# Kernel tuning notes

Hardware: AMD Instinct MI355X
Metric: run time of the kernel (lower is better)

## Reference

```python
import jax, jax.numpy as jnp
import numpy as np

HIDDEN = 128
N_RBF = 32
LMAX = 2
N_NODES = 10000
DEG = 8  # each node has DEG outgoing (and DEG incoming) edges on a ring


def _build_graph():
    src = np.repeat(np.arange(N_NODES, dtype=np.int64), DEG)
    offs = np.tile(np.arange(1, DEG + 1, dtype=np.int64), N_NODES)
    dst = (src + offs) % N_NODES
    keys = src * N_NODES + dst
    order = np.argsort(keys)
    src2, dst2 = src[order], dst[order]  # e2 sorted by key (searchsorted invariant)
    e1_to_e2 = np.empty_like(order)
    e1_to_e2[order] = np.arange(order.size)
    return src, dst, src2, dst2, e1_to_e2


def setup_inputs() -> dict:
    key = jax.random.key(0)
    ks = jax.random.split(key, 12)
    src1, dst1, src2, dst2, e1_to_e2 = _build_graph()
    E1, E2 = src1.size, src2.size
    in_dim = 6 * HIDDEN + 3 * N_RBF + 1  # 865

    def lin(k, fi, fo):
        kw, kb = jax.random.split(k)
        s = 1.0 / np.sqrt(fi)
        return (jax.random.uniform(kw, (fi, fo), minval=-s, maxval=s),
                jax.random.uniform(kb, (fo,), minval=-s, maxval=s))

    w1, b1 = lin(ks[0], in_dim, HIDDEN)
    w2, b2 = lin(ks[1], HIDDEN, HIDDEN)
    wgw, bgw = lin(ks[2], HIDDEN, HIDDEN)
    wgt, bgt = lin(ks[3], HIDDEN, HIDDEN)
    return {
        "t_e2": jax.random.normal(ks[4], (E2, HIDDEN), dtype=jnp.float32),
        "h": jax.random.normal(ks[5], (N_NODES, HIDDEN), dtype=jnp.float32),
        "edge_index1": jnp.asarray(np.stack([src1, dst1])),
        "edge_index2": jnp.asarray(np.stack([src2, dst2])),
        "e1_to_e2": jnp.asarray(e1_to_e2),
        "dist_e1": jax.random.uniform(ks[6], (E1,), dtype=jnp.float32),
        "dist_e2": jax.random.uniform(ks[7], (E2,), dtype=jnp.float32),
        "rbf_e1": jax.random.normal(ks[8], (E1, N_RBF), dtype=jnp.float32),
        "rbf_e2": jax.random.normal(ks[9], (E2, N_RBF), dtype=jnp.float32),
        "sph_e1": jax.random.normal(ks[10], (E1, LMAX + 1), dtype=jnp.float32),
        "num_nodes": N_NODES,
        "w1": w1, "b1": b1, "w2": w2, "b2": b2,
        "wgw": wgw, "bgw": bgw, "wgt": wgt, "bgt": bgt,
    }


def _wedge_indices(edge_index1, edge_index2, num_nodes):
    """Host-side (numpy, vectorized) wedge construction: for every center node k,
    all (incoming edge i->k, outgoing edge k->j) pairs with i != j, kept only when
    (i, j) itself is an edge in e2 (looked up by sorted key search)."""
    src1 = np.asarray(edge_index1[0]); dst1 = np.asarray(edge_index1[1])
    src2 = np.asarray(edge_index2[0]); dst2 = np.asarray(edge_index2[1])
    nz = src1 != dst1  # drop self-loops
    s, d = src1[nz], dst1[nz]
    eid = np.nonzero(nz)[0]
    out_deg = np.bincount(s, minlength=num_nodes)
    out_order = np.argsort(s, kind="stable")  # filtered-edge positions grouped by src
    out_ptr = np.concatenate([np.zeros(1, np.int64), np.cumsum(out_deg)])
    reps = out_deg[d]  # each incoming edge pairs with out_deg[center] outgoing edges
    total = int(reps.sum())
    if total == 0:
        z = np.zeros(0, np.int64)
        return z, z, z, z, z, z
    starts = np.cumsum(reps) - reps
    local = np.arange(total) - np.repeat(starts, reps)
    kj_f = out_order[np.repeat(out_ptr[d], reps) + local]
    i = np.repeat(s, reps)
    k = np.repeat(d, reps)
    eik = np.repeat(eid, reps)
    j = d[kj_f]
    ekj = eid[kj_f]
    m = i != j
    i, k, j, eik, ekj = i[m], k[m], j[m], eik[m], ekj[m]
    e2_keys = src2.astype(np.int64) * num_nodes + dst2
    pk = i.astype(np.int64) * num_nodes + j
    pos = np.searchsorted(e2_keys, pk)
    posc = np.minimum(pos, e2_keys.size - 1)
    valid = (pos < e2_keys.size) & (e2_keys[posc] == pk)
    return i[valid], k[valid], j[valid], eik[valid], ekj[valid], posc[valid]


def reference(t_e2, h, edge_index1, edge_index2, e1_to_e2, dist_e1, dist_e2,
              rbf_e1, rbf_e2, sph_e1, num_nodes,
              w1, b1, w2, b2, wgw, bgw, wgt, bgt):
    i, k, j, eik, ekj, eij = _wedge_indices(edge_index1, edge_index2, int(num_nodes))
    if i.size == 0:
        return t_e2
    i, k, j = jnp.asarray(i), jnp.asarray(k), jnp.asarray(j)
    eik, ekj, eij = jnp.asarray(eik), jnp.asarray(ekj), jnp.asarray(eij)
    e1e2 = jnp.asarray(e1_to_e2)
    # wedge geometric features (wedge_use_high_degree=False -> l=1 contraction only)
    c_feat = (sph_e1[eik, 1] * sph_e1[ekj, 1])[:, None]           # [W, 1]
    g = jnp.concatenate([rbf_e1[eik], rbf_e1[ekj], rbf_e2[eij], c_feat], axis=-1)
    rho_in = jnp.concatenate([t_e2[e1e2[eik]], t_e2[e1e2[ekj]], t_e2[eij],
                              h[i], h[k], h[j], g], axis=-1)       # [W, 865]
    msg = jax.nn.silu(rho_in @ w1 + b1) @ w2 + b2                  # [W, H]
    m = jax.ops.segment_sum(msg, eij, num_segments=t_e2.shape[0])  # [E2, H]
    return t_e2 + jax.nn.sigmoid(m @ wgw + bgw) * jnp.tanh(t_e2 @ wgt + bgt)
```

## Files before the change

kernel.cpp:

```cpp
#include <hip/hip_runtime.h>
#include <math.h>

typedef unsigned short u16;
typedef unsigned int u32;
typedef __bf16 bf16x8 __attribute__((ext_vector_type(8)));
typedef float f32x4 __attribute__((ext_vector_type(4)));

__device__ __forceinline__ float bf2f(u16 v){ union{u32 u;float f;}c; c.u=((u32)v)<<16; return c.f; }
__device__ __forceinline__ u16 f2bf(float f){ union{__bf16 h; u16 u;}c; c.h=(__bf16)f; return c.u; }
__device__ __forceinline__ u32 pk2(float a, float b){
  union{ __bf16 h[2]; u32 u; }c; c.h[0]=(__bf16)a; c.h[1]=(__bf16)b; return c.u;
}
__device__ __forceinline__ uint4 ld8f(const float* p){
  float4 x = ((const float4*)p)[0];
  float4 y = ((const float4*)p)[1];
  uint4 r; r.x=pk2(x.x,x.y); r.y=pk2(x.z,x.w); r.z=pk2(y.x,y.y); r.w=pk2(y.z,y.w);
  return r;
}
__device__ __forceinline__ float fsilu(float x){
  return x*__builtin_amdgcn_rcpf(1.f+__expf(-x));
}

__global__ void k_setup_all(const int* __restrict__ e1_to_e2,
                            const float* __restrict__ rbf_e1,
                            const float* __restrict__ sph_e1,
                            u16* __restrict__ rbf1p, float* __restrict__ sph_c, int E1,
                            const int* __restrict__ src2, int* __restrict__ out_ptr,
                            int Nn, int E2,
                            const float* __restrict__ w1,
                            u16* __restrict__ W0T, u16* __restrict__ W1T,
                            u16* __restrict__ W2T,
                            const float* __restrict__ w2, const float* __restrict__ wgw,
                            const float* __restrict__ wgt, const float* __restrict__ b2,
                            u16* __restrict__ WcT, u16* __restrict__ WgtT,
                            float* __restrict__ bc2,
                            int nb0, int nb1, int nb2) {
  const int b = blockIdx.x, t = threadIdx.x;
  if (b < nb0) {
    int e = b*256 + t;
    if (e >= E1) return;
    int f = e1_to_e2[e];
    sph_c[f] = sph_e1[e*3+1];
    const float* s = rbf_e1 + (size_t)e*32;
    uint4* d = (uint4*)(rbf1p + (size_t)f*32);
    d[0]=ld8f(s); d[1]=ld8f(s+8); d[2]=ld8f(s+16); d[3]=ld8f(s+24);
  } else if (b < nb1) {
    int n = (b-nb0)*256 + t;
    if (n > Nn) return;
    int lo=0, hi=E2;
    while (lo<hi){ int m=(lo+hi)>>1; if (src2[m]<n) lo=m+1; else hi=m; }
    out_ptr[n]=lo;
  } else if (b < nb2) {
    int id = (b-nb1)*256 + t;
    if (id < 128*416) {
      int n = id/416, k = id - n*416;
      int row = (k<128)? k : (k<256)? 384+(k-128) : (k<384)? 512+(k-256) : 768+(k-384);
      W0T[id] = f2bf(w1[row*128+n]);
    } else if (id < 128*(416+288)) {
      int id2 = id - 128*416;
      int n = id2/288, k = id2 - n*288;
      int row = (k<128)? 128+k : (k<256)? 640+(k-128) : 800+(k-256);
      W1T[id2] = f2bf(w1[row*128+n]);
    } else if (id < 128*864) {
      int id2 = id - 128*704;
      int n = id2/160, k = id2 - n*160;
      int row = (k<128)? 256+k : 832+(k-128);
      W2T[id2] = f2bf(w1[row*128+n]);
    }
  } else {
    int id = (b-nb2)*256 + t;
    if (id < 16384) {
      int n = id&127, k = id>>7;
      float s = 0.f;
      for (int r=0;r<128;r++) s += w2[k*128+r]*wgw[r*128+n];
      WcT[n*128+k] = f2bf(s);
      WgtT[n*128+k] = f2bf(wgt[k*128+n]);
    } else if (id < 16384+128) {
      int n = id-16384;
      float s = 0.f;
      for (int r=0;r<128;r++) s += b2[r]*wgw[r*128+n];
      bc2[n] = s;
    }
  }
}

__global__ __launch_bounds__(256, 8)
void k_wedge(const int* __restrict__ src2, const int* __restrict__ dst2,
             const int* __restrict__ out_ptr, const float* __restrict__ sph_c,
             const u16* __restrict__ Q1, const u16* __restrict__ Q2,
             const u16* __restrict__ P3, const float* __restrict__ w1,
             u16* __restrict__ S, int* __restrict__ cnt, int E2) {
  int gw = (int)((blockIdx.x*256 + threadIdx.x) >> 6);
  int lane = threadIdx.x & 63;
  if (gw >= E2) return;
  int i = src2[gw], j = dst2[gw];
  int f = 0, lo = 0; float cf = 0.f; bool valid = false;
  if (lane < 8) {
    int ff = out_ptr[i] + lane;
    if (ff < out_ptr[i+1]) {
      int k = dst2[ff];
      int l = out_ptr[k], hh = out_ptr[k+1], h0 = hh;
      while (l<hh){ int m=(l+hh)>>1; if (dst2[m]<j) l=m+1; else hh=m; }
      if (l<h0 && dst2[l]==j){ valid=true; f=ff; lo=l; cf=sph_c[ff]*sph_c[l]; }
    }
  }
  unsigned long long mask = __ballot(valid);
  const int nw = __popcll(mask);
  if (lane==0) cnt[gw] = nw;
  u32 p3u = ((const u32*)(P3 + (size_t)gw*128))[lane];
  float p30 = bf2f((u16)(p3u&0xffff)), p31 = bf2f((u16)(p3u>>16));
  float2 wv = ((const float2*)(w1 + 864*128))[lane];
  const u32* q1b = (const u32*)Q1;
  const u32* q2b = (const u32*)Q2;

  u32 xa[8], ya[8]; float ca[8];
  unsigned long long m2 = mask;
  #pragma unroll
  for (int s=0; s<8; s++) {
    if (s < nw) {
      int b = __ffsll((long long)m2)-1; m2 &= m2-1;
      int fA = __builtin_amdgcn_readlane(f, b);
      int lA = __builtin_amdgcn_readlane(lo, b);
      ca[s] = __int_as_float(__builtin_amdgcn_readlane(__float_as_int(cf), b));
      xa[s] = q1b[((size_t)(u32)fA<<6) + lane];
      ya[s] = q2b[((size_t)(u32)lA<<6) + lane];
    }
  }

  float a0=0.f, a1=0.f;
  #pragma unroll
  for (int s=0; s<8; s++) {
    if (s < nw) {
      float b0 = fmaf(ca[s], wv.x, p30);
      float b1 = fmaf(ca[s], wv.y, p31);
      float x0 = b0 + bf2f((u16)(xa[s]&0xffff)) + bf2f((u16)(ya[s]&0xffff));
      float x1 = b1 + bf2f((u16)(xa[s]>>16))    + bf2f((u16)(ya[s]>>16));
      a0 += fsilu(x0);
      a1 += fsilu(x1);
    }
  }
  ((u32*)(S + (size_t)gw*128))[lane] = pk2(a0, a1);
}

struct GArgs {
  const float* t_f32; const float* h; const float* rbf_e2;
  const u16* rbf1p; const u16* Asrc;
  const int* src2; const int* dst2; const int* cnt;
  const u16* B0; const u16* B1; const u16* B2;
  const u16* Bmat; const u16* Bmat2;
  const float* b1; const float* bgw; const float* bgt; const float* bc2;
  u16* out0; u16* out1; u16* out2;
  float* outf;
  int M;
};

__global__ __launch_bounds__(256, 2)
void k_gemm0(GArgs a) {
  const int nwg = gridDim.x;
  const int id  = blockIdx.x;
  const int xcd = id & 7, idx = id >> 3;
  const int q = nwg >> 3, r = nwg & 7;
  const int w = (xcd < r ? xcd*(q+1) : r*(q+1) + (xcd-r)*q) + idx;
  const int bm = w/3, bn = w - bm*3;

  __shared__ u16 As[128*40];
  __shared__ u16 Bs[128*40];
  const int tid = threadIdx.x;
  const int lane = tid & 63, wave = tid >> 6;
  const int wm = wave >> 1, wn = wave & 1;
  const int quad = lane >> 4, l16 = lane & 15;

  const int part = tid & 3;
  const int ra = tid >> 2;
  const int rb = ra + 64;
  long fa = (long)bm*128 + ra;
  long fb = (long)bm*128 + rb;
  if (fa >= a.M) fa = a.M-1;
  if (fb >= a.M) fb = a.M-1;
  int sa=0, sb=0, da=0, db=0;
  if (bn==0) { sa=a.src2[fa]; sb=a.src2[fb]; }
  if (bn<2)  { da=a.dst2[fa]; db=a.dst2[fb]; }

  const u16* Bp = (bn==0)? a.B0 : (bn==1)? a.B1 : a.B2;
  const int NK = (bn==0)? 13 : (bn==1)? 9 : 5;
  const int KT = NK*32;

  f32x4 acc[4][4] = {};
  for (int ks=0; ks<NK; ks++) {
    const int kb = ks*32;
    uint4 va, vb;
    if (ks<4)                    { va = ld8f(a.t_f32 + fa*128 + kb + part*8);
                                   vb = ld8f(a.t_f32 + fb*128 + kb + part*8); }
    else if (bn==0 && ks<8)      { va = ld8f(a.h + (long)sa*128 + (kb-128) + part*8);
                                   vb = ld8f(a.h + (long)sb*128 + (kb-128) + part*8); }
    else if (bn==0 && ks<12)     { va = ld8f(a.h + (long)da*128 + (kb-256) + part*8);
                                   vb = ld8f(a.h + (long)db*128 + (kb-256) + part*8); }
    else if (bn==1 && ks<8)      { va = ld8f(a.h + (long)da*128 + (kb-128) + part*8);
                                   vb = ld8f(a.h + (long)db*128 + (kb-128) + part*8); }
    else if (bn==2)              { va = ld8f(a.rbf_e2 + fa*32 + part*8);
                                   vb = ld8f(a.rbf_e2 + fb*32 + part*8); }
    else                         { va = *(const uint4*)(a.rbf1p + fa*32 + part*8);
                                   vb = *(const uint4*)(a.rbf1p + fb*32 + part*8); }
    uint4 wa = *(const uint4*)(Bp + (long)ra*KT + kb + part*8);
    uint4 wb = *(const uint4*)(Bp + (long)rb*KT + kb + part*8);
    __syncthreads();
    *(uint4*)(As + ra*40 + part*8) = va;
    *(uint4*)(As + rb*40 + part*8) = vb;
    *(uint4*)(Bs + ra*40 + part*8) = wa;
    *(uint4*)(Bs + rb*40 + part*8) = wb;
    __syncthreads();
    bf16x8 af[4], bfr[4];
    #pragma unroll
    for (int t=0;t<4;t++) {
      af[t]  = *(const bf16x8*)(As + (wm*64 + t*16 + l16)*40 + quad*8);
      bfr[t] = *(const bf16x8*)(Bs + (wn*64 + t*16 + l16)*40 + quad*8);
    }
    #pragma unroll
    for (int tm=0;tm<4;tm++)
      #pragma unroll
      for (int tn=0;tn<4;tn++)
        acc[tm][tn] = __builtin_amdgcn_mfma_f32_16x16x32_bf16(af[tm], bfr[tn], acc[tm][tn], 0,0,0);
  }

  #pragma unroll
  for (int tm=0;tm<4;tm++) {
    const int rloc = wm*64 + tm*16 + quad*4;
    #pragma unroll
    for (int r=0;r<4;r++) {
      long row = (long)bm*128 + rloc + r;
      if (row >= a.M) continue;
      #pragma unroll
      for (int tn=0;tn<4;tn++) {
        const int col = wn*64 + tn*16 + l16;
        float v = acc[tm][tn][r];
        u16* dst = (bn==0)? a.out0 : (bn==1)? a.out1 : a.out2;
        if (bn==2) v += a.b1[col];
        dst[row*128 + col] = f2bf(v);
      }
    }
  }
}

__global__ __launch_bounds__(256, 2)
void k_gemm12(GArgs a) {
  __shared__ u16 As[128*40];
  __shared__ u16 Bs[128*40];
  const int tid = threadIdx.x;
  const int bm = blockIdx.x;
  const int lane = tid & 63, wave = tid >> 6;
  const int wm = wave >> 1, wn = wave & 1;
  const int quad = lane >> 4, l16 = lane & 15;

  const int part = tid & 3;
  const int ra = tid >> 2;
  const int rb = ra + 64;
  long fa = (long)bm*128 + ra;
  long fb = (long)bm*128 + rb;
  if (fa >= a.M) fa = a.M-1;
  if (fb >= a.M) fb = a.M-1;

  f32x4 acc1[4][4] = {};
  f32x4 acc2[4][4] = {};
  for (int ks=0; ks<4; ks++) {
    const int kb = ks*32;
    uint4 va = *(const uint4*)(a.Asrc + fa*128 + kb + part*8);
    uint4 vb = *(const uint4*)(a.Asrc + fb*128 + kb + part*8);
    uint4 wa = *(const uint4*)(a.Bmat + (long)ra*128 + kb + part*8);
    uint4 wbv= *(const uint4*)(a.Bmat + (long)rb*128 + kb + part*8);
    __syncthreads();
    *(uint4*)(As + ra*40 + part*8) = va;
    *(uint4*)(As + rb*40 + part*8) = vb;
    *(uint4*)(Bs + ra*40 + part*8) = wa;
    *(uint4*)(Bs + rb*40 + part*8) = wbv;
    __syncthreads();
    bf16x8 af[4], bfr[4];
    #pragma unroll
    for (int t=0;t<4;t++) {
      af[t]  = *(const bf16x8*)(As + (wm*64 + t*16 + l16)*40 + quad*8);
      bfr[t] = *(const bf16x8*)(Bs + (wn*64 + t*16 + l16)*40 + quad*8);
    }
    #pragma unroll
    for (int tm=0;tm<4;tm++)
      #pragma unroll
      for (int tn=0;tn<4;tn++)
        acc1[tm][tn] = __builtin_amdgcn_mfma_f32_16x16x32_bf16(af[tm], bfr[tn], acc1[tm][tn], 0,0,0);
  }
  for (int ks=0; ks<4; ks++) {
    const int kb = ks*32;
    uint4 va = ld8f(a.t_f32 + fa*128 + kb + part*8);
    uint4 vb = ld8f(a.t_f32 + fb*128 + kb + part*8);
    uint4 wa = *(const uint4*)(a.Bmat2 + (long)ra*128 + kb + part*8);
    uint4 wbv= *(const uint4*)(a.Bmat2 + (long)rb*128 + kb + part*8);
    __syncthreads();
    *(uint4*)(As + ra*40 + part*8) = va;
    *(uint4*)(As + rb*40 + part*8) = vb;
    *(uint4*)(Bs + ra*40 + part*8) = wa;
    *(uint4*)(Bs + rb*40 + part*8) = wbv;
    __syncthreads();
    bf16x8 af[4], bfr[4];
    #pragma unroll
    for (int t=0;t<4;t++) {
      af[t]  = *(const bf16x8*)(As + (wm*64 + t*16 + l16)*40 + quad*8);
      bfr[t] = *(const bf16x8*)(Bs + (wn*64 + t*16 + l16)*40 + quad*8);
    }
    #pragma unroll
    for (int tm=0;tm<4;tm++)
      #pragma unroll
      for (int tn=0;tn<4;tn++)
        acc2[tm][tn] = __builtin_amdgcn_mfma_f32_16x16x32_bf16(af[tm], bfr[tn], acc2[tm][tn], 0,0,0);
  }

  #pragma unroll
  for (int tm=0;tm<4;tm++) {
    const int rloc = wm*64 + tm*16 + quad*4;
    #pragma unroll
    for (int r=0;r<4;r++) {
      long row = (long)bm*128 + rloc + r;
      if (row >= a.M) continue;
      #pragma unroll
      for (int tn=0;tn<4;tn++) {
        const int col = wn*64 + tn*16 + l16;
        float u = acc1[tm][tn][r] + (float)a.cnt[row]*a.bc2[col] + a.bgw[col];
        float g = __builtin_amdgcn_rcpf(1.f+__expf(-u));
        float vv = acc2[tm][tn][r] + a.bgt[col];
        float th = 1.f - 2.f*__builtin_amdgcn_rcpf(__expf(2.f*vv)+1.f);
        float t  = a.t_f32[row*128+col];
        a.outf[row*128+col] = t + g*th;
      }
    }
  }
}

extern "C" void kernel_launch(void* const* d_in, const int* in_sizes, int n_in,
                              void* d_out, int out_size, void* d_ws, size_t ws_size,
                              hipStream_t stream) {
  const float* t_e2  = (const float*)d_in[0];
  const float* h     = (const float*)d_in[1];
  const int* ei2     = (const int*)d_in[3];
  const int* e1_to_e2 = (const int*)d_in[4];
  const float* rbf_e1 = (const float*)d_in[7];
  const float* rbf_e2 = (const float*)d_in[8];
  const float* sph_e1 = (const float*)d_in[9];
  const float* w1  = (const float*)d_in[11];
  const float* b1  = (const float*)d_in[12];
  const float* w2  = (const float*)d_in[13];
  const float* b2  = (const float*)d_in[14];
  const float* wgw = (const float*)d_in[15];
  const float* bgw = (const float*)d_in[16];
  const float* wgt = (const float*)d_in[17];
  const float* bgt = (const float*)d_in[18];

  const int E2 = in_sizes[0]/128;
  const int Nn = in_sizes[1]/128;
  const int E1 = in_sizes[5];
  const int* src2 = ei2;
  const int* dst2 = ei2 + E2;

  char* p = (char*)d_ws;
  u16* Q1 = (u16*)p;       p += (size_t)E2*128*2;
  u16* Q2 = (u16*)p;       p += (size_t)E2*128*2;
  u16* P3 = (u16*)p;       p += (size_t)E2*128*2;
  u16* rbf1p = (u16*)p;    p += (size_t)E2*32*2;
  u16* W0T = (u16*)p;      p += (size_t)128*416*2;
  u16* W1T = (u16*)p;      p += (size_t)128*288*2;
  u16* W2T = (u16*)p;      p += (size_t)128*160*2;
  u16* WcT   = (u16*)p;    p += (size_t)128*128*2;
  u16* WgtT  = (u16*)p;    p += (size_t)128*128*2;
  float* sph_c = (float*)p; p += (size_t)E2*4;
  float* bc2   = (float*)p; p += 512;
  int* out_ptr = (int*)p;   p += (((size_t)(Nn+1)*4 + 63)/64)*64;
  int* cnt     = (int*)p;   p += (size_t)E2*4;
  u16* S = P3;

  const int nb_edges = (E1+255)/256;
  const int nb_ptr   = (Nn+1+255)/256;
  const int nb_w     = (128*864+255)/256;
  const int nb_small = (16512+255)/256;
  const int nb0 = nb_edges;
  const int nb1 = nb0 + nb_ptr;
  const int nb2 = nb1 + nb_w;
  const int nbT = nb2 + nb_small;
  k_setup_all<<<nbT, 256, 0, stream>>>(e1_to_e2, rbf_e1, sph_e1, rbf1p, sph_c, E1,
                                       src2, out_ptr, Nn, E2,
                                       w1, W0T, W1T, W2T,
                                       w2, wgw, wgt, b2,
                                       WcT, WgtT, bc2,
                                       nb0, nb1, nb2);

  const int Mb = (E2+127)/128;
  {
    GArgs a = {};
    a.t_f32=t_e2; a.h=h; a.rbf1p=rbf1p; a.rbf_e2=rbf_e2;
    a.src2=src2; a.dst2=dst2;
    a.B0=W0T; a.B1=W1T; a.B2=W2T; a.b1=b1;
    a.out0=Q1; a.out1=Q2; a.out2=P3; a.M=E2;
    k_gemm0<<<Mb*3, 256, 0, stream>>>(a);
  }
  k_wedge<<<(E2+3)/4, 256, 0, stream>>>(src2, dst2, out_ptr, sph_c,
                                        Q1, Q2, P3, w1, S, cnt, E2);
  {
    GArgs a = {};
    a.Asrc=S; a.cnt=cnt; a.Bmat=WcT; a.Bmat2=WgtT;
    a.bgw=bgw; a.bgt=bgt; a.bc2=bc2; a.t_f32=t_e2;
    a.outf=(float*)d_out; a.M=E2;
    k_gemm12<<<Mb, 256, 0, stream>>>(a);
  }
}
```

Baseline: 281.1 us.

## Double-buffer LDS tiles in gemm kernels to overlap global loads with MFMA

Both GEMM kernels now use two LDS buffers per operand, prefetching the next K-slice into registers while MFMAs consume the current slice, then writing it to the alternate buffer. This cuts one barrier per iteration and hides global load latency behind compute. k_gemm0 also raises launch_bounds min blocks from 2 to 4, which may pressure registers given the 64 accumulator floats plus prefetch registers, and doubled LDS (40KB per block) could limit occupancy.

```diff
diff --git a/kernel.cpp b/kernel.cpp
--- a/kernel.cpp
+++ b/kernel.cpp
@@ -154,7 +154,18 @@
   int M;
 };
 
-__global__ __launch_bounds__(256, 2)
+__device__ __forceinline__ uint4 ldA(const GArgs& a, int bn, int ks, long f,
+                                     int s, int d, int part) {
+  const int kb = ks*32;
+  if (ks<4)                return ld8f(a.t_f32 + f*128 + kb + part*8);
+  if (bn==0 && ks<8)       return ld8f(a.h + (long)s*128 + (kb-128) + part*8);
+  if (bn==0 && ks<12)      return ld8f(a.h + (long)d*128 + (kb-256) + part*8);
+  if (bn==1 && ks<8)       return ld8f(a.h + (long)d*128 + (kb-128) + part*8);
+  if (bn==2)               return ld8f(a.rbf_e2 + f*32 + part*8);
+  return *(const uint4*)(a.rbf1p + f*32 + part*8);
+}
+
+__global__ __launch_bounds__(256, 4)
 void k_gemm0(GArgs a) {
   const int nwg = gridDim.x;
   const int id  = blockIdx.x;
@@ -163,8 +174,8 @@
   const int w = (xcd < r ? xcd*(q+1) : r*(q+1) + (xcd-r)*q) + idx;
   const int bm = w/3, bn = w - bm*3;
 
-  __shared__ u16 As[128*40];
-  __shared__ u16 Bs[128*40];
+  __shared__ u16 As[2][128*40];
+  __shared__ u16 Bs[2][128*40];
   const int tid = threadIdx.x;
   const int lane = tid & 63, wave = tid >> 6;
   const int wm = wave >> 1, wn = wave & 1;
@@ -185,41 +196,43 @@
   const int NK = (bn==0)? 13 : (bn==1)? 9 : 5;
   const int KT = NK*32;
 
+  uint4 va = ldA(a,bn,0,fa,sa,da,part);
+  uint4 vb = ldA(a,bn,0,fb,sb,db,part);
+  uint4 wa = *(const uint4*)(Bp + (long)ra*KT + part*8);
+  uint4 wb = *(const uint4*)(Bp + (long)rb*KT + part*8);
+  *(uint4*)(As[0] + ra*40 + part*8) = va;
+  *(uint4*)(As[0] + rb*40 + part*8) = vb;
+  *(uint4*)(Bs[0] + ra*40 + part*8) = wa;
+  *(uint4*)(Bs[0] + rb*40 + part*8) = wb;
+
   f32x4 acc[4][4] = {};
   for (int ks=0; ks<NK; ks++) {
-    const int kb = ks*32;
-    uint4 va, vb;
-    if (ks<4)                    { va = ld8f(a.t_f32 + fa*128 + kb + part*8);
-                                   vb = ld8f(a.t_f32 + fb*128 + kb + part*8); }
-    else if (bn==0 && ks<8)      { va = ld8f(a.h + (long)sa*128 + (kb-128) + part*8);
-                                   vb = ld8f(a.h + (long)sb*128 + (kb-128) + part*8); }
-    else if (bn==0 && ks<12)     { va = ld8f(a.h + (long)da*128 + (kb-256) + part*8);
-                                   vb = ld8f(a.h + (long)db*128 + (kb-256) + part*8); }
-    else if (bn==1 && ks<8)      { va = ld8f(a.h + (long)da*128 + (kb-128) + part*8);
-                                   vb = ld8f(a.h + (long)db*128 + (kb-128) + part*8); }
-    else if (bn==2)              { va = ld8f(a.rbf_e2 + fa*32 + part*8);
-                                   vb = ld8f(a.rbf_e2 + fb*32 + part*8); }
-    else                         { va = *(const uint4*)(a.rbf1p + fa*32 + part*8);
-                                   vb = *(const uint4*)(a.rbf1p + fb*32 + part*8); }
-    uint4 wa = *(const uint4*)(Bp + (long)ra*KT + kb + part*8);
-    uint4 wb = *(const uint4*)(Bp + (long)rb*KT + kb + part*8);
+    const int cur = ks & 1;
     __syncthreads();
-    *(uint4*)(As + ra*40 + part*8) = va;
-    *(uint4*)(As + rb*40 + part*8) = vb;
-    *(uint4*)(Bs + ra*40 + part*8) = wa;
-    *(uint4*)(Bs + rb*40 + part*8) = wb;
-    __syncthreads();
+    if (ks+1 < NK) {
+      const int kb = (ks+1)*32;
+      va = ldA(a,bn,ks+1,fa,sa,da,part);
+      vb = ldA(a,bn,ks+1,fb,sb,db,part);
+      wa = *(const uint4*)(Bp + (long)ra*KT + kb + part*8);
+      wb = *(const uint4*)(Bp + (long)rb*KT + kb + part*8);
+    }
     bf16x8 af[4], bfr[4];
     #pragma unroll
     for (int t=0;t<4;t++) {
-      af[t]  = *(const bf16x8*)(As + (wm*64 + t*16 + l16)*40 + quad*8);
-      bfr[t] = *(const bf16x8*)(Bs + (wn*64 + t*16 + l16)*40 + quad*8);
+      af[t]  = *(const bf16x8*)(As[cur] + (wm*64 + t*16 + l16)*40 + quad*8);
+      bfr[t] = *(const bf16x8*)(Bs[cur] + (wn*64 + t*16 + l16)*40 + quad*8);
     }
     #pragma unroll
     for (int tm=0;tm<4;tm++)
       #pragma unroll
       for (int tn=0;tn<4;tn++)
         acc[tm][tn] = __builtin_amdgcn_mfma_f32_16x16x32_bf16(af[tm], bfr[tn], acc[tm][tn], 0,0,0);
+    if (ks+1 < NK) {
+      *(uint4*)(As[cur^1] + ra*40 + part*8) = va;
+      *(uint4*)(As[cur^1] + rb*40 + part*8) = vb;
+      *(uint4*)(Bs[cur^1] + ra*40 + part*8) = wa;
+      *(uint4*)(Bs[cur^1] + rb*40 + part*8) = wb;
+    }
   }
 
   #pragma unroll
@@ -243,8 +256,8 @@
 
 __global__ __launch_bounds__(256, 2)
 void k_gemm12(GArgs a) {
-  __shared__ u16 As[128*40];
-  __shared__ u16 Bs[128*40];
+  __shared__ u16 As[2][128*40];
+  __shared__ u16 Bs[2][128*40];
   const int tid = threadIdx.x;
   const int bm = blockIdx.x;
   const int lane = tid & 63, wave = tid >> 6;
@@ -261,53 +274,83 @@
 
   f32x4 acc1[4][4] = {};
   f32x4 acc2[4][4] = {};
-  for (int ks=0; ks<4; ks++) {
-    const int kb = ks*32;
-    uint4 va = *(const uint4*)(a.Asrc + fa*128 + kb + part*8);
-    uint4 vb = *(const uint4*)(a.Asrc + fb*128 + kb + part*8);
-    uint4 wa = *(const uint4*)(a.Bmat + (long)ra*128 + kb + part*8);
-    uint4 wbv= *(const uint4*)(a.Bmat + (long)rb*128 + kb + part*8);
-    __syncthreads();
-    *(uint4*)(As + ra*40 + part*8) = va;
-    *(uint4*)(As + rb*40 + part*8) = vb;
-    *(uint4*)(Bs + ra*40 + part*8) = wa;
-    *(uint4*)(Bs + rb*40 + part*8) = wbv;
-    __syncthreads();
-    bf16x8 af[4], bfr[4];
-    #pragma unroll
-    for (int t=0;t<4;t++) {
-      af[t]  = *(const bf16x8*)(As + (wm*64 + t*16 + l16)*40 + quad*8);
-      bfr[t] = *(const bf16x8*)(Bs + (wn*64 + t*16 + l16)*40 + quad*8);
-    }
-    #pragma unroll
-    for (int tm=0;tm<4;tm++)
-      #pragma unroll
-      for (int tn=0;tn<4;tn++)
-        acc1[tm][tn] = __builtin_amdgcn_mfma_f32_16x16x32_bf16(af[tm], bfr[tn], acc1[tm][tn], 0,0,0);
-  }
-  for (int ks=0; ks<4; ks++) {
-    const int kb = ks*32;
-    uint4 va = ld8f(a.t_f32 + fa*128 + kb + part*8);
-    uint4 vb = ld8f(a.t_f32 + fb*128 + kb + part*8);
-    uint4 wa = *(const uint4*)(a.Bmat2 + (long)ra*128 + kb + part*8);
-    uint4 wbv= *(const uint4*)(a.Bmat2 + (long)rb*128 + kb + part*8);
-    __syncthreads();
-    *(uint4*)(As + ra*40 + part*8) = va;
-    *(uint4*)(As + rb*40 + part*8) = vb;
-    *(uint4*)(Bs + ra*40 + part*8) = wa;
-    *(uint4*)(Bs + rb*40 + part*8) = wbv;
-    __syncthreads();
-    bf16x8 af[4], bfr[4];
-    #pragma unroll
-    for (int t=0;t<4;t++) {
-      af[t]  = *(const bf16x8*)(As + (wm*64 + t*16 + l16)*40 + quad*8);
-      bfr[t] = *(const bf16x8*)(Bs + (wn*64 + t*16 + l16)*40 + quad*8);
-    }
-    #pragma unroll
-    for (int tm=0;tm<4;tm++)
-      #pragma unroll
-      for (int tn=0;tn<4;tn++)
-        acc2[tm][tn] = __builtin_amdgcn_mfma_f32_16x16x32_bf16(af[tm], bfr[tn], acc2[tm][tn], 0,0,0);
+
+  {
+    uint4 va = *(const uint4*)(a.Asrc + fa*128 + part*8);
+    uint4 vb = *(const uint4*)(a.Asrc + fb*128 + part*8);
+    uint4 wa = *(const uint4*)(a.Bmat + (long)ra*128 + part*8);
+    uint4 wbv= *(const uint4*)(a.Bmat + (long)rb*128 + part*8);
+    *(uint4*)(As[0] + ra*40 + part*8) = va;
+    *(uint4*)(As[0] + rb*40 + part*8) = vb;
+    *(uint4*)(Bs[0] + ra*40 + part*8) = wa;
+    *(uint4*)(Bs[0] + rb*40 + part*8) = wbv;
+    for (int ks=0; ks<4; ks++) {
+      const int cur = ks & 1;
+      __syncthreads();
+      if (ks+1 < 4) {
+        const int kb = (ks+1)*32;
+        va = *(const uint4*)(a.Asrc + fa*128 + kb + part*8);
+        vb = *(const uint4*)(a.Asrc + fb*128 + kb + part*8);
+        wa = *(const uint4*)(a.Bmat + (long)ra*128 + kb + part*8);
+        wbv= *(const uint4*)(a.Bmat + (long)rb*128 + kb + part*8);
+      }
+      bf16x8 af[4], bfr[4];
+      #pragma unroll
+      for (int t=0;t<4;t++) {
+        af[t]  = *(const bf16x8*)(As[cur] + (wm*64 + t*16 + l16)*40 + quad*8);
+        bfr[t] = *(const bf16x8*)(Bs[cur] + (wn*64 + t*16 + l16)*40 + quad*8);
+      }
+      #pragma unroll
+      for (int tm=0;tm<4;tm++)
+        #pragma unroll
+        for (int tn=0;tn<4;tn++)
+          acc1[tm][tn] = __builtin_amdgcn_mfma_f32_16x16x32_bf16(af[tm], bfr[tn], acc1[tm][tn], 0,0,0);
+      if (ks+1 < 4) {
+        *(uint4*)(As[cur^1] + ra*40 + part*8) = va;
+        *(uint4*)(As[cur^1] + rb*40 + part*8) = vb;
+        *(uint4*)(Bs[cur^1] + ra*40 + part*8) = wa;
+        *(uint4*)(Bs[cur^1] + rb*40 + part*8) = wbv;
+      }
+    }
+  }
+  __syncthreads();
+  {
+    uint4 va = ld8f(a.t_f32 + fa*128 + part*8);
+    uint4 vb = ld8f(a.t_f32 + fb*128 + part*8);
+    uint4 wa = *(const uint4*)(a.Bmat2 + (long)ra*128 + part*8);
+    uint4 wbv= *(const uint4*)(a.Bmat2 + (long)rb*128 + part*8);
+    *(uint4*)(As[0] + ra*40 + part*8) = va;
+    *(uint4*)(As[0] + rb*40 + part*8) = vb;
+    *(uint4*)(Bs[0] + ra*40 + part*8) = wa;
+    *(uint4*)(Bs[0] + rb*40 + part*8) = wbv;
+    for (int ks=0; ks<4; ks++) {
+      const int cur = ks & 1;
+      __syncthreads();
+      if (ks+1 < 4) {
+        const int kb = (ks+1)*32;
+        va = ld8f(a.t_f32 + fa*128 + kb + part*8);
+        vb = ld8f(a.t_f32 + fb*128 + kb + part*8);
+        wa = *(const uint4*)(a.Bmat2 + (long)ra*128 + kb + part*8);
+        wbv= *(const uint4*)(a.Bmat2 + (long)rb*128 + kb + part*8);
+      }
+      bf16x8 af[4], bfr[4];
+      #pragma unroll
+      for (int t=0;t<4;t++) {
+        af[t]  = *(const bf16x8*)(As[cur] + (wm*64 + t*16 + l16)*40 + quad*8);
+        bfr[t] = *(const bf16x8*)(Bs[cur] + (wn*64 + t*16 + l16)*40 + quad*8);
+      }
+      #pragma unroll
+      for (int tm=0;tm<4;tm++)
+        #pragma unroll
+        for (int tn=0;tn<4;tn++)
+          acc2[tm][tn] = __builtin_amdgcn_mfma_f32_16x16x32_bf16(af[tm], bfr[tn], acc2[tm][tn], 0,0,0);
+      if (ks+1 < 4) {
+        *(uint4*)(As[cur^1] + ra*40 + part*8) = va;
+        *(uint4*)(As[cur^1] + rb*40 + part*8) = vb;
+        *(uint4*)(Bs[cur^1] + ra*40 + part*8) = wa;
+        *(uint4*)(Bs[cur^1] + rb*40 + part*8) = wbv;
+      }
+    }
   }
 
   #pragma unroll
```

New measurement: 319.8 us. 1.14x slower.

## Load MFMA fragments directly from global memory, dropping LDS staging in GEMMs

Applied to the files above, without the earlier changes.

The GEMM kernels now skip shared-memory staging and __syncthreads. Each wave loads its bf16x8 A and B fragments straight from global memory, and k_gemm0 double-buffers them in registers across k-steps. h and rbf_e2 are pre-converted to bf16 in the setup kernel so the fragment loads are direct vector reads. k_gemm0 is also templated per column block so the branch logic is resolved at compile time. The cost is redundant global and L2 traffic, since each wave re-reads rows that LDS staging used to share, plus higher register pressure and an extra conversion pass in setup.

```diff
diff --git a/kernel.cpp b/kernel.cpp
--- a/kernel.cpp
+++ b/kernel.cpp
@@ -17,6 +17,7 @@
   uint4 r; r.x=pk2(x.x,x.y); r.y=pk2(x.z,x.w); r.z=pk2(y.x,y.y); r.w=pk2(y.z,y.w);
   return r;
 }
+__device__ __forceinline__ bf16x8 u4tob(uint4 v){ union{uint4 u; bf16x8 b;}c; c.u=v; return c.b; }
 __device__ __forceinline__ float fsilu(float x){
   return x*__builtin_amdgcn_rcpf(1.f+__expf(-x));
 }
@@ -34,7 +35,9 @@
                             const float* __restrict__ wgt, const float* __restrict__ b2,
                             u16* __restrict__ WcT, u16* __restrict__ WgtT,
                             float* __restrict__ bc2,
-                            int nb0, int nb1, int nb2) {
+                            const float* __restrict__ h, u16* __restrict__ h_bf,
+                            const float* __restrict__ rbf_e2, u16* __restrict__ rbf2p,
+                            int nb0, int nb1, int nb2, int nb3, int nb4) {
   const int b = blockIdx.x, t = threadIdx.x;
   if (b < nb0) {
     int e = b*256 + t;
@@ -67,7 +70,7 @@
       int row = (k<128)? 256+k : 832+(k-128);
       W2T[id2] = f2bf(w1[row*128+n]);
     }
-  } else {
+  } else if (b < nb3) {
     int id = (b-nb2)*256 + t;
     if (id < 16384) {
       int n = id&127, k = id>>7;
@@ -81,6 +84,12 @@
       for (int r=0;r<128;r++) s += b2[r]*wgw[r*128+n];
       bc2[n] = s;
     }
+  } else if (b < nb4) {
+    int id = (b-nb3)*256 + t;
+    if (id < Nn*16) ((uint4*)h_bf)[id] = ld8f(h + (size_t)id*8);
+  } else {
+    int id = (b-nb4)*256 + t;
+    if (id < E2*4) ((uint4*)rbf2p)[id] = ld8f(rbf_e2 + (size_t)id*8);
   }
 }
 
@@ -143,7 +152,7 @@
 }
 
 struct GArgs {
-  const float* t_f32; const float* h; const float* rbf_e2;
+  const float* t_f32; const u16* h_bf; const u16* rbf2p;
   const u16* rbf1p; const u16* Asrc;
   const int* src2; const int* dst2; const int* cnt;
   const u16* B0; const u16* B1; const u16* B2;
@@ -154,6 +163,90 @@
   int M;
 };
 
+template<int BN>
+__device__ __forceinline__ bf16x8 ldAfrag(const GArgs& a, int ks, long row,
+                                          int hs_, int hd_, int off) {
+  if (ks<4) return u4tob(ld8f(a.t_f32 + row*128 + ks*32 + off));
+  if (BN==0) {
+    if (ks<8)  return *(const bf16x8*)(a.h_bf + (long)hs_*128 + (ks-4)*32 + off);
+    if (ks<12) return *(const bf16x8*)(a.h_bf + (long)hd_*128 + (ks-8)*32 + off);
+    return *(const bf16x8*)(a.rbf1p + row*32 + off);
+  } else if (BN==1) {
+    if (ks<8)  return *(const bf16x8*)(a.h_bf + (long)hd_*128 + (ks-4)*32 + off);
+    return *(const bf16x8*)(a.rbf1p + row*32 + off);
+  } else {
+    return *(const bf16x8*)(a.rbf2p + row*32 + off);
+  }
+}
+
+template<int BN>
+__device__ __forceinline__ void gemm0_body(const GArgs& a, int bm,
+                                           int wm, int wn, int quad, int l16) {
+  constexpr int NK = (BN==0)?13:((BN==1)?9:5);
+  constexpr int KT = NK*32;
+  const int off = quad*8;
+  long rowA[4]; int hs[4], hd[4]; const u16* bp[4];
+  const u16* Bp = (BN==0)? a.B0 : (BN==1)? a.B1 : a.B2;
+  #pragma unroll
+  for (int t=0;t<4;t++) {
+    long r = (long)bm*128 + wm*64 + t*16 + l16; if (r >= a.M) r = a.M-1;
+    rowA[t]=r;
+    hs[t] = (BN==0)? a.src2[r] : 0;
+    hd[t] = (BN<2)?  a.dst2[r] : 0;
+    bp[t] = Bp + (long)(wn*64 + t*16 + l16)*KT + off;
+  }
+  f32x4 acc[4][4] = {};
+  bf16x8 A0[4], B0v[4], A1[4], B1v[4];
+
+  #pragma unroll
+  for (int t=0;t<4;t++) { A0[t]=ldAfrag<BN>(a,0,rowA[t],hs[t],hd[t],off);
+                          B0v[t]=*(const bf16x8*)(bp[t]); }
+  #pragma unroll
+  for (int ks=0; ks<NK; ks++) {
+    if ((ks&1)==0) {
+      if (ks+1<NK) {
+        #pragma unroll
+        for (int t=0;t<4;t++){ A1[t]=ldAfrag<BN>(a,ks+1,rowA[t],hs[t],hd[t],off);
+                               B1v[t]=*(const bf16x8*)(bp[t]+(ks+1)*32); }
+      }
+      #pragma unroll
+      for (int tm=0;tm<4;tm++)
+        #pragma unroll
+        for (int tn=0;tn<4;tn++)
+          acc[tm][tn] = __builtin_amdgcn_mfma_f32_16x16x32_bf16(A0[tm], B0v[tn], acc[tm][tn], 0,0,0);
+    } else {
+      if (ks+1<NK) {
+        #pragma unroll
+        for (int t=0;t<4;t++){ A0[t]=ldAfrag<BN>(a,ks+1,rowA[t],hs[t],hd[t],off);
+                               B0v[t]=*(const bf16x8*)(bp[t]+(ks+1)*32); }
+      }
+      #pragma unroll
+      for (int tm=0;tm<4;tm++)
+        #pragma unroll
+        for (int tn=0;tn<4;tn++)
+          acc[tm][tn] = __builtin_amdgcn_mfma_f32_16x16x32_bf16(A1[tm], B1v[tn], acc[tm][tn], 0,0,0);
+    }
+  }
+
+  u16* dst = (BN==0)? a.out0 : (BN==1)? a.out1 : a.out2;
+  #pragma unroll
+  for (int tm=0;tm<4;tm++) {
+    const int rloc = wm*64 + tm*16 + quad*4;
+    #pragma unroll
+    for (int r=0;r<4;r++) {
+      long row = (long)bm*128 + rloc + r;
+      if (row >= a.M) continue;
+      #pragma unroll
+      for (int tn=0;tn<4;tn++) {
+        const int col = wn*64 + tn*16 + l16;
+        float v = acc[tm][tn][r];
+        if (BN==2) v += a.b1[col];
+        dst[row*128 + col] = f2bf(v);
+      }
+    }
+  }
+}
+
 __global__ __launch_bounds__(256, 2)
 void k_gemm0(GArgs a) {
   const int nwg = gridDim.x;
@@ -162,122 +255,43 @@
   const int q = nwg >> 3, r = nwg & 7;
   const int w = (xcd < r ? xcd*(q+1) : r*(q+1) + (xcd-r)*q) + idx;
   const int bm = w/3, bn = w - bm*3;
-
-  __shared__ u16 As[128*40];
-  __shared__ u16 Bs[128*40];
   const int tid = threadIdx.x;
   const int lane = tid & 63, wave = tid >> 6;
   const int wm = wave >> 1, wn = wave & 1;
   const int quad = lane >> 4, l16 = lane & 15;
-
-  const int part = tid & 3;
-  const int ra = tid >> 2;
-  const int rb = ra + 64;
-  long fa = (long)bm*128 + ra;
-  long fb = (long)bm*128 + rb;
-  if (fa >= a.M) fa = a.M-1;
-  if (fb >= a.M) fb = a.M-1;
-  int sa=0, sb=0, da=0, db=0;
-  if (bn==0) { sa=a.src2[fa]; sb=a.src2[fb]; }
-  if (bn<2)  { da=a.dst2[fa]; db=a.dst2[fb]; }
-
-  const u16* Bp = (bn==0)? a.B0 : (bn==1)? a.B1 : a.B2;
-  const int NK = (bn==0)? 13 : (bn==1)? 9 : 5;
-  const int KT = NK*32;
-
-  f32x4 acc[4][4] = {};
-  for (int ks=0; ks<NK; ks++) {
-    const int kb = ks*32;
-    uint4 va, vb;
-    if (ks<4)                    { va = ld8f(a.t_f32 + fa*128 + kb + part*8);
-                                   vb = ld8f(a.t_f32 + fb*128 + kb + part*8); }
-    else if (bn==0 && ks<8)      { va = ld8f(a.h + (long)sa*128 + (kb-128) + part*8);
-                                   vb = ld8f(a.h + (long)sb*128 + (kb-128) + part*8); }
-    else if (bn==0 && ks<12)     { va = ld8f(a.h + (long)da*128 + (kb-256) + part*8);
-                                   vb = ld8f(a.h + (long)db*128 + (kb-256) + part*8); }
-    else if (bn==1 && ks<8)      { va = ld8f(a.h + (long)da*128 + (kb-128) + part*8);
-                                   vb = ld8f(a.h + (long)db*128 + (kb-128) + part*8); }
-    else if (bn==2)              { va = ld8f(a.rbf_e2 + fa*32 + part*8);
-                                   vb = ld8f(a.rbf_e2 + fb*32 + part*8); }
-    else                         { va = *(const uint4*)(a.rbf1p + fa*32 + part*8);
-                                   vb = *(const uint4*)(a.rbf1p + fb*32 + part*8); }
-    uint4 wa = *(const uint4*)(Bp + (long)ra*KT + kb + part*8);
-    uint4 wb = *(const uint4*)(Bp + (long)rb*KT + kb + part*8);
-    __syncthreads();
-    *(uint4*)(As + ra*40 + part*8) = va;
-    *(uint4*)(As + rb*40 + part*8) = vb;
-    *(uint4*)(Bs + ra*40 + part*8) = wa;
-    *(uint4*)(Bs + rb*40 + part*8) = wb;
-    __syncthreads();
-    bf16x8 af[4], bfr[4];
-    #pragma unroll
-    for (int t=0;t<4;t++) {
-      af[t]  = *(const bf16x8*)(As + (wm*64 + t*16 + l16)*40 + quad*8);
-      bfr[t] = *(const bf16x8*)(Bs + (wn*64 + t*16 + l16)*40 + quad*8);
-    }
-    #pragma unroll
-    for (int tm=0;tm<4;tm++)
-      #pragma unroll
-      for (int tn=0;tn<4;tn++)
-        acc[tm][tn] = __builtin_amdgcn_mfma_f32_16x16x32_bf16(af[tm], bfr[tn], acc[tm][tn], 0,0,0);
-  }
-
-  #pragma unroll
-  for (int tm=0;tm<4;tm++) {
-    const int rloc = wm*64 + tm*16 + quad*4;
-    #pragma unroll
-    for (int r=0;r<4;r++) {
-      long row = (long)bm*128 + rloc + r;
-      if (row >= a.M) continue;
-      #pragma unroll
-      for (int tn=0;tn<4;tn++) {
-        const int col = wn*64 + tn*16 + l16;
-        float v = acc[tm][tn][r];
-        u16* dst = (bn==0)? a.out0 : (bn==1)? a.out1 : a.out2;
-        if (bn==2) v += a.b1[col];
-        dst[row*128 + col] = f2bf(v);
-      }
-    }
-  }
+  if (bn==0)      gemm0_body<0>(a, bm, wm, wn, quad, l16);
+  else if (bn==1) gemm0_body<1>(a, bm, wm, wn, quad, l16);
+  else            gemm0_body<2>(a, bm, wm, wn, quad, l16);
 }
 
 __global__ __launch_bounds__(256, 2)
 void k_gemm12(GArgs a) {
-  __shared__ u16 As[128*40];
-  __shared__ u16 Bs[128*40];
+  const int bm = blockIdx.x;
   const int tid = threadIdx.x;
-  const int bm = blockIdx.x;
   const int lane = tid & 63, wave = tid >> 6;
   const int wm = wave >> 1, wn = wave & 1;
   const int quad = lane >> 4, l16 = lane & 15;
-
-  const int part = tid & 3;
-  const int ra = tid >> 2;
-  const int rb = ra + 64;
-  long fa = (long)bm*128 + ra;
-  long fb = (long)bm*128 + rb;
-  if (fa >= a.M) fa = a.M-1;
-  if (fb >= a.M) fb = a.M-1;
-
+  const int off = quad*8;
+
+  long rowA[4]; const u16 *bc[4], *bg[4];
+  #pragma unroll
+  for (int t=0;t<4;t++) {
+    long r = (long)bm*128 + wm*64 + t*16 + l16; if (r >= a.M) r = a.M-1;
+    rowA[t]=r;
+    long rowB = (long)(wn*64 + t*16 + l16)*128;
+    bc[t] = a.Bmat  + rowB + off;
+    bg[t] = a.Bmat2 + rowB + off;
+  }
   f32x4 acc1[4][4] = {};
   f32x4 acc2[4][4] = {};
+
+  #pragma unroll
   for (int ks=0; ks<4; ks++) {
-    const int kb = ks*32;
-    uint4 va = *(const uint4*)(a.Asrc + fa*128 + kb + part*8);
-    uint4 vb = *(const uint4*)(a.Asrc + fb*128 + kb + part*8);
-    uint4 wa = *(const uint4*)(a.Bmat + (long)ra*128 + kb + part*8);
-    uint4 wbv= *(const uint4*)(a.Bmat + (long)rb*128 + kb + part*8);
-    __syncthreads();
-    *(uint4*)(As + ra*40 + part*8) = va;
-    *(uint4*)(As + rb*40 + part*8) = vb;
-    *(uint4*)(Bs + ra*40 + part*8) = wa;
-    *(uint4*)(Bs + rb*40 + part*8) = wbv;
-    __syncthreads();
     bf16x8 af[4], bfr[4];
     #pragma unroll
     for (int t=0;t<4;t++) {
-      af[t]  = *(const bf16x8*)(As + (wm*64 + t*16 + l16)*40 + quad*8);
-      bfr[t] = *(const bf16x8*)(Bs + (wn*64 + t*16 + l16)*40 + quad*8);
+      af[t]  = *(const bf16x8*)(a.Asrc + rowA[t]*128 + ks*32 + off);
+      bfr[t] = *(const bf16x8*)(bc[t] + ks*32);
     }
     #pragma unroll
     for (int tm=0;tm<4;tm++)
@@ -285,23 +299,13 @@
       for (int tn=0;tn<4;tn++)
         acc1[tm][tn] = __builtin_amdgcn_mfma_f32_16x16x32_bf16(af[tm], bfr[tn], acc1[tm][tn], 0,0,0);
   }
+  #pragma unroll
   for (int ks=0; ks<4; ks++) {
-    const int kb = ks*32;
-    uint4 va = ld8f(a.t_f32 + fa*128 + kb + part*8);
-    uint4 vb = ld8f(a.t_f32 + fb*128 + kb + part*8);
-    uint4 wa = *(const uint4*)(a.Bmat2 + (long)ra*128 + kb + part*8);
-    uint4 wbv= *(const uint4*)(a.Bmat2 + (long)rb*128 + kb + part*8);
-    __syncthreads();
-    *(uint4*)(As + ra*40 + part*8) = va;
-    *(uint4*)(As + rb*40 + part*8) = vb;
-    *(uint4*)(Bs + ra*40 + part*8) = wa;
-    *(uint4*)(Bs + rb*40 + part*8) = wbv;
-    __syncthreads();
     bf16x8 af[4], bfr[4];
     #pragma unroll
     for (int t=0;t<4;t++) {
-      af[t]  = *(const bf16x8*)(As + (wm*64 + t*16 + l16)*40 + quad*8);
-      bfr[t] = *(const bf16x8*)(Bs + (wn*64 + t*16 + l16)*40 + quad*8);
+      af[t]  = u4tob(ld8f(a.t_f32 + rowA[t]*128 + ks*32 + off));
+      bfr[t] = *(const bf16x8*)(bg[t] + ks*32);
     }
     #pragma unroll
     for (int tm=0;tm<4;tm++)
@@ -361,6 +365,8 @@
   u16* Q2 = (u16*)p;       p += (size_t)E2*128*2;
   u16* P3 = (u16*)p;       p += (size_t)E2*128*2;
   u16* rbf1p = (u16*)p;    p += (size_t)E2*32*2;
+  u16* rbf2p = (u16*)p;    p += (size_t)E2*32*2;
+  u16* h_bf  = (u16*)p;    p += (size_t)Nn*128*2;
   u16* W0T = (u16*)p;      p += (size_t)128*416*2;
   u16* W1T = (u16*)p;      p += (size_t)128*288*2;
   u16* W2T = (u16*)p;      p += (size_t)128*160*2;
@@ -376,21 +382,26 @@
   const int nb_ptr   = (Nn+1+255)/256;
   const int nb_w     = (128*864+255)/256;
   const int nb_small = (16512+255)/256;
+  const int nb_hbf   = (Nn*16+255)/256;
+  const int nb_rbf2  = (E2*4+255)/256;
   const int nb0 = nb_edges;
   const int nb1 = nb0 + nb_ptr;
   const int nb2 = nb1 + nb_w;
-  const int nbT = nb2 + nb_small;
+  const int nb3 = nb2 + nb_small;
+  const int nb4 = nb3 + nb_hbf;
+  const int nbT = nb4 + nb_rbf2;
   k_setup_all<<<nbT, 256, 0, stream>>>(e1_to_e2, rbf_e1, sph_e1, rbf1p, sph_c, E1,
                                        src2, out_ptr, Nn, E2,
                                        w1, W0T, W1T, W2T,
                                        w2, wgw, wgt, b2,
                                        WcT, WgtT, bc2,
-                                       nb0, nb1, nb2);
+                                       h, h_bf, rbf_e2, rbf2p,
+                                       nb0, nb1, nb2, nb3, nb4);
 
   const int Mb = (E2+127)/128;
   {
     GArgs a = {};
-    a.t_f32=t_e2; a.h=h; a.rbf1p=rbf1p; a.rbf_e2=rbf_e2;
+    a.t_f32=t_e2; a.h_bf=h_bf; a.rbf1p=rbf1p; a.rbf2p=rbf2p;
     a.src2=src2; a.dst2=dst2;
     a.B0=W0T; a.B1=W1T; a.B2=W2T; a.b1=b1;
     a.out0=Q1; a.out1=Q2; a.out2=P3; a.M=E2;
```

Result: slower. 330.8 us (+17.7%).

## Precompute node-level h projections once per node and gather in edge GEMM epilogue

Applied to the files above, without the earlier changes.

The h[i], h[k], h[j] contributions to the first MLP layer are now projected once per node (10000 rows) in a new small GEMM kernel, instead of being gathered and multiplied for every edge (80000 rows). The edge GEMM shrinks to a uniform K=160 for all three column blocks and adds the gathered per-node projections in its epilogue through a larger shared-memory staging buffer. This cuts redundant MFMA work and strided h gathers, at the cost of an extra kernel launch, extra workspace, bf16 rounding of the node projections before summation, and higher LDS use per block (64 KB), which may lower occupancy.

```diff
diff --git a/kernel.cpp b/kernel.cpp
--- a/kernel.cpp
+++ b/kernel.cpp
@@ -27,9 +27,7 @@
                             u16* __restrict__ rbf1p, float* __restrict__ sph_c, int E1,
                             const int* __restrict__ src2, int* __restrict__ out_ptr,
                             int Nn, int E2,
-                            const float* __restrict__ w1,
-                            u16* __restrict__ W0T, u16* __restrict__ W1T,
-                            u16* __restrict__ W2T,
+                            const float* __restrict__ w1, u16* __restrict__ Wall,
                             const float* __restrict__ w2, const float* __restrict__ wgw,
                             const float* __restrict__ wgt, const float* __restrict__ b2,
                             u16* __restrict__ WcT, u16* __restrict__ WgtT,
@@ -52,20 +50,22 @@
     out_ptr[n]=lo;
   } else if (b < nb2) {
     int id = (b-nb1)*256 + t;
-    if (id < 128*416) {
-      int n = id/416, k = id - n*416;
-      int row = (k<128)? k : (k<256)? 384+(k-128) : (k<384)? 512+(k-256) : 768+(k-384);
-      W0T[id] = f2bf(w1[row*128+n]);
-    } else if (id < 128*(416+288)) {
-      int id2 = id - 128*416;
-      int n = id2/288, k = id2 - n*288;
-      int row = (k<128)? 128+k : (k<256)? 640+(k-128) : 800+(k-256);
-      W1T[id2] = f2bf(w1[row*128+n]);
-    } else if (id < 128*864) {
-      int id2 = id - 128*704;
-      int n = id2/160, k = id2 - n*160;
-      int row = (k<128)? 256+k : 832+(k-128);
-      W2T[id2] = f2bf(w1[row*128+n]);
+    if (id < 61440) {
+      int m = id / 20480;
+      int r2 = id - m*20480;
+      int n = r2 / 160, k = r2 - n*160;
+      int row;
+      if (m==0)      row = (k<128)? k       : 768+(k-128);
+      else if (m==1) row = (k<128)? 128+k   : 800+(k-128);
+      else           row = (k<128)? 256+k   : 832+(k-128);
+      Wall[id] = f2bf(w1[row*128+n]);
+    } else if (id < 110592) {
+      int idh = id - 61440;
+      int m = idh >> 14;
+      int r2 = idh & 16383;
+      int n = r2 >> 7, k = r2 & 127;
+      int base = 384 + m*128;
+      Wall[id] = f2bf(w1[(base+k)*128+n]);
     }
   } else {
     int id = (b-nb2)*256 + t;
@@ -80,6 +80,65 @@
       float s = 0.f;
       for (int r=0;r<128;r++) s += b2[r]*wgw[r*128+n];
       bc2[n] = s;
+    }
+  }
+}
+
+__global__ __launch_bounds__(256, 2)
+void k_gemmH(const float* __restrict__ h, const u16* __restrict__ WH,
+             u16* __restrict__ Hout, int Nn) {
+  const int bm = blockIdx.x, bn = blockIdx.y;
+  const u16* Bp = WH + bn*16384;
+  u16* dst = Hout + (size_t)bn*Nn*128;
+  __shared__ u16 As[128*40];
+  __shared__ u16 Bs[128*40];
+  const int tid = threadIdx.x;
+  const int lane = tid & 63, wave = tid >> 6;
+  const int wm = wave >> 1, wn = wave & 1;
+  const int quad = lane >> 4, l16 = lane & 15;
+  const int part = tid & 3;
+  const int ra = tid >> 2;
+  const int rb = ra + 64;
+  long fa = (long)bm*128 + ra; if (fa >= Nn) fa = Nn-1;
+  long fb = (long)bm*128 + rb; if (fb >= Nn) fb = Nn-1;
+
+  f32x4 acc[4][4] = {};
+  for (int ks=0; ks<4; ks++) {
+    const int kb = ks*32;
+    uint4 va = ld8f(h + fa*128 + kb + part*8);
+    uint4 vb = ld8f(h + fb*128 + kb + part*8);
+    uint4 wa = *(const uint4*)(Bp + (long)ra*128 + kb + part*8);
+    uint4 wb = *(const uint4*)(Bp + (long)rb*128 + kb + part*8);
+    __syncthreads();
+    *(uint4*)(As + ra*40 + part*8) = va;
+    *(uint4*)(As + rb*40 + part*8) = vb;
+    *(uint4*)(Bs + ra*40 + part*8) = wa;
+    *(uint4*)(Bs + rb*40 + part*8) = wb;
+    __syncthreads();
+    bf16x8 af[4], bfr[4];
+    #pragma unroll
+    for (int t=0;t<4;t++) {
+      af[t]  = *(const bf16x8*)(As + (wm*64 + t*16 + l16)*40 + quad*8);
+      bfr[t] = *(const bf16x8*)(Bs + (wn*64 + t*16 + l16)*40 + quad*8);
+    }
+    #pragma unroll
+    for (int tm=0;tm<4;tm++)
+      #pragma unroll
+      for (int tn=0;tn<4;tn++)
+        acc[tm][tn] = __builtin_amdgcn_mfma_f32_16x16x32_bf16(af[tm], bfr[tn], acc[tm][tn], 0,0,0);
+  }
+  #pragma unroll
+  for (int tm=0;tm<4;tm++) {
+    const int rloc = wm*64 + tm*16 + quad*4;
+    #pragma unroll
+    for (int r=0;r<4;r++) {
+      long row = (long)bm*128 + rloc + r;
+      if (row >= Nn) continue;
+      #pragma unroll
+      for (int tn=0;tn<4;tn++) {
+        const int col = wn*64 + tn*16 + l16;
+        dst[row*128 + col] = f2bf(acc[tm][tn][r]);
+      }
     }
   }
 }
@@ -143,10 +202,11 @@
 }
 
 struct GArgs {
-  const float* t_f32; const float* h; const float* rbf_e2;
+  const float* t_f32; const float* rbf_e2;
   const u16* rbf1p; const u16* Asrc;
   const int* src2; const int* dst2; const int* cnt;
   const u16* B0; const u16* B1; const u16* B2;
+  const u16* Hi; const u16* Hk; const u16* Hj;
   const u16* Bmat; const u16* Bmat2;
   const float* b1; const float* bgw; const float* bgt; const float* bc2;
   u16* out0; u16* out1; u16* out2;
@@ -163,8 +223,9 @@
   const int w = (xcd < r ? xcd*(q+1) : r*(q+1) + (xcd-r)*q) + idx;
   const int bm = w/3, bn = w - bm*3;
 
-  __shared__ u16 As[128*40];
-  __shared__ u16 Bs[128*40];
+  __shared__ u16 sm[32768];
+  u16* As = sm;
+  u16* Bs = sm + 5120;
   const int tid = threadIdx.x;
   const int lane = tid & 63, wave = tid >> 6;
   const int wm = wave >> 1, wn = wave & 1;
@@ -177,30 +238,20 @@
   long fb = (long)bm*128 + rb;
   if (fa >= a.M) fa = a.M-1;
   if (fb >= a.M) fb = a.M-1;
-  int sa=0, sb=0, da=0, db=0;
-  if (bn==0) { sa=a.src2[fa]; sb=a.src2[fb]; }
-  if (bn<2)  { da=a.dst2[fa]; db=a.dst2[fb]; }
 
   const u16* Bp = (bn==0)? a.B0 : (bn==1)? a.B1 : a.B2;
-  const int NK = (bn==0)? 13 : (bn==1)? 9 : 5;
-  const int KT = NK*32;
+  constexpr int KT = 160;
 
   f32x4 acc[4][4] = {};
-  for (int ks=0; ks<NK; ks++) {
+  for (int ks=0; ks<5; ks++) {
     const int kb = ks*32;
     uint4 va, vb;
-    if (ks<4)                    { va = ld8f(a.t_f32 + fa*128 + kb + part*8);
-                                   vb = ld8f(a.t_f32 + fb*128 + kb + part*8); }
-    else if (bn==0 && ks<8)      { va = ld8f(a.h + (long)sa*128 + (kb-128) + part*8);
-                                   vb = ld8f(a.h + (long)sb*128 + (kb-128) + part*8); }
-    else if (bn==0 && ks<12)     { va = ld8f(a.h + (long)da*128 + (kb-256) + part*8);
-                                   vb = ld8f(a.h + (long)db*128 + (kb-256) + part*8); }
-    else if (bn==1 && ks<8)      { va = ld8f(a.h + (long)da*128 + (kb-128) + part*8);
-                                   vb = ld8f(a.h + (long)db*128 + (kb-128) + part*8); }
-    else if (bn==2)              { va = ld8f(a.rbf_e2 + fa*32 + part*8);
-                                   vb = ld8f(a.rbf_e2 + fb*32 + part*8); }
-    else                         { va = *(const uint4*)(a.rbf1p + fa*32 + part*8);
-                                   vb = *(const uint4*)(a.rbf1p + fb*32 + part*8); }
+    if (ks<4)        { va = ld8f(a.t_f32 + fa*128 + kb + part*8);
+                       vb = ld8f(a.t_f32 + fb*128 + kb + part*8); }
+    else if (bn<2)   { va = *(const uint4*)(a.rbf1p + fa*32 + part*8);
+                       vb = *(const uint4*)(a.rbf1p + fb*32 + part*8); }
+    else             { va = ld8f(a.rbf_e2 + fa*32 + part*8);
+                       vb = ld8f(a.rbf_e2 + fb*32 + part*8); }
     uint4 wa = *(const uint4*)(Bp + (long)ra*KT + kb + part*8);
     uint4 wb = *(const uint4*)(Bp + (long)rb*KT + kb + part*8);
     __syncthreads();
@@ -222,6 +273,27 @@
         acc[tm][tn] = __builtin_amdgcn_mfma_f32_16x16x32_bf16(af[tm], bfr[tn], acc[tm][tn], 0,0,0);
   }
 
+  if (bn < 2) {
+    __syncthreads();
+    #pragma unroll
+    for (int c=0;c<8;c++) {
+      int idx2 = tid + c*256;
+      int row = idx2 >> 4, ch = idx2 & 15;
+      long fr = (long)bm*128 + row;
+      if (fr >= a.M) fr = a.M-1;
+      if (bn==0) {
+        int s = a.src2[fr], d = a.dst2[fr];
+        *(uint4*)(&sm[row*128 + ch*8])         = *(const uint4*)(a.Hi + (long)s*128 + ch*8);
+        *(uint4*)(&sm[16384 + row*128 + ch*8]) = *(const uint4*)(a.Hk + (long)d*128 + ch*8);
+      } else {
+        int d = a.dst2[fr];
+        *(uint4*)(&sm[row*128 + ch*8])         = *(const uint4*)(a.Hj + (long)d*128 + ch*8);
+      }
+    }
+    __syncthreads();
+  }
+
+  u16* dst = (bn==0)? a.out0 : (bn==1)? a.out1 : a.out2;
   #pragma unroll
   for (int tm=0;tm<4;tm++) {
     const int rloc = wm*64 + tm*16 + quad*4;
@@ -229,12 +301,14 @@
     for (int r=0;r<4;r++) {
       long row = (long)bm*128 + rloc + r;
       if (row >= a.M) continue;
+      const int rl = rloc + r;
       #pragma unroll
       for (int tn=0;tn<4;tn++) {
         const int col = wn*64 + tn*16 + l16;
         float v = acc[tm][tn][r];
-        u16* dst = (bn==0)? a.out0 : (bn==1)? a.out1 : a.out2;
-        if (bn==2) v += a.b1[col];
+        if (bn==0)      v += bf2f(sm[rl*128+col]) + bf2f(sm[16384+rl*128+col]);
+        else if (bn==1) v += bf2f(sm[rl*128+col]);
+        else            v += a.b1[col];
         dst[row*128 + col] = f2bf(v);
       }
     }
@@ -361,9 +435,8 @@
   u16* Q2 = (u16*)p;       p += (size_t)E2*128*2;
   u16* P3 = (u16*)p;       p += (size_t)E2*128*2;
   u16* rbf1p = (u16*)p;    p += (size_t)E2*32*2;
-  u16* W0T = (u16*)p;      p += (size_t)128*416*2;
-  u16* W1T = (u16*)p;      p += (size_t)128*288*2;
-  u16* W2T = (u16*)p;      p += (size_t)128*160*2;
+  u16* Hout  = (u16*)p;    p += (size_t)3*Nn*128*2;
+  u16* Wall  = (u16*)p;    p += (size_t)110592*2;
   u16* WcT   = (u16*)p;    p += (size_t)128*128*2;
   u16* WgtT  = (u16*)p;    p += (size_t)128*128*2;
   float* sph_c = (float*)p; p += (size_t)E2*4;
@@ -371,10 +444,11 @@
   int* out_ptr = (int*)p;   p += (((size_t)(Nn+1)*4 + 63)/64)*64;
   int* cnt     = (int*)p;   p += (size_t)E2*4;
   u16* S = P3;
+  u16* Hi = Hout, *Hk = Hout + (size_t)Nn*128, *Hj = Hout + (size_t)2*Nn*128;
 
   const int nb_edges = (E1+255)/256;
   const int nb_ptr   = (Nn+1+255)/256;
-  const int nb_w     = (128*864+255)/256;
+  const int nb_w     = (110592+255)/256;
   const int nb_small = (16512+255)/256;
   const int nb0 = nb_edges;
   const int nb1 = nb0 + nb_ptr;
@@ -382,17 +456,20 @@
   const int nbT = nb2 + nb_small;
   k_setup_all<<<nbT, 256, 0, stream>>>(e1_to_e2, rbf_e1, sph_e1, rbf1p, sph_c, E1,
                                        src2, out_ptr, Nn, E2,
-                                       w1, W0T, W1T, W2T,
-                                       w2, wgw, wgt, b2,
+                                       w1, Wall, w2, wgw, wgt, b2,
                                        WcT, WgtT, bc2,
                                        nb0, nb1, nb2);
+
+  const int Mh = (Nn+127)/128;
+  k_gemmH<<<dim3(Mh,3), 256, 0, stream>>>(h, Wall + 61440, Hout, Nn);
 
   const int Mb = (E2+127)/128;
   {
     GArgs a = {};
-    a.t_f32=t_e2; a.h=h; a.rbf1p=rbf1p; a.rbf_e2=rbf_e2;
+    a.t_f32=t_e2; a.rbf_e2=rbf_e2; a.rbf1p=rbf1p;
     a.src2=src2; a.dst2=dst2;
-    a.B0=W0T; a.B1=W1T; a.B2=W2T; a.b1=b1;
+    a.B0=Wall; a.B1=Wall+20480; a.B2=Wall+40960;
+    a.Hi=Hi; a.Hk=Hk; a.Hj=Hj; a.b1=b1;
     a.out0=Q1; a.out1=Q2; a.out2=P3; a.M=E2;
     k_gemm0<<<Mb*3, 256, 0, stream>>>(a);
   }
```

Result: slower. 329.4 us (+17.2%).
